# Performance work log

Hardware: AMD Instinct MI355X
Metric: run time of the kernel (lower is better)

Reference implementation:

```python
import jax, jax.numpy as jnp
import numpy as np

B, E, W_WORDS, V = 512, 512, 64, 32000
H = 10 * E  # dense hidden = embedding_size * 10


def setup_inputs() -> dict:
    key = jax.random.key(0)
    ks = jax.random.split(key, 16)
    u = lambda k, shp: jax.random.uniform(ks[k], shp, jnp.float32, -0.05, 0.05)
    n = lambda k, shp: jax.random.normal(ks[k], shp, jnp.float32)
    return {
        "y": n(0, (B, E)),
        "state": n(1, (B, E)),
        "encode": n(2, (B, W_WORDS, E)),
        # Bahdanau attention weights (W4 unused in forward, omitted)
        "aW1": u(3, (1, E)),
        "aW2": u(4, (W_WORDS, E)),
        "aW3": u(5, (W_WORDS, E)),
        # Keras GRU (reset_after=True): kernel, recurrent_kernel, bias[2, 3E]
        "gk": u(6, (E, 3 * E)),
        "grk": u(7, (E, 3 * E)),
        "gb": u(8, (2, 3 * E)),
        # Dense stack
        "w1": u(9, (3 * E, H)), "b1": jnp.zeros((H,), jnp.float32),
        "w2": u(10, (H, H)), "b2": jnp.zeros((H,), jnp.float32),
        "w3": u(11, (H, V)), "b3": jnp.zeros((V,), jnp.float32),
    }


def _attention(query, value, aW1, aW2, aW3):
    # einsum('bi,ci->bi', query, W1) with c==1  ->  query * W1[0]
    rq = query * aW1[0]                       # [B, E]
    rv = value * aW2                          # [B, W, E] (broadcast over batch)
    s = jnp.tanh(rq[:, None, :] * rv)         # [B, W, E]
    scores = jnp.sum(s * aW3, axis=-1)        # [B, W]
    a = jax.nn.softmax(scores, axis=-1)       # [B, W]
    return jnp.einsum('bw,bwe->be', a, value)  # context [B, E]


def _gru(seq, gk, grk, gb):
    # seq: [T, B, E]; keras GRU defaults: tanh / sigmoid, reset_after=True, h0=0
    bi, br = gb[0], gb[1]

    def step(h, x):
        xz, xr, xh = jnp.split(x @ gk + bi, 3, axis=-1)
        rz, rr, rh = jnp.split(h @ grk + br, 3, axis=-1)
        z = jax.nn.sigmoid(xz + rz)
        r = jax.nn.sigmoid(xr + rr)
        hh = jnp.tanh(xh + r * rh)
        return z * h + (1.0 - z) * hh, None

    h0 = jnp.zeros(seq.shape[1:], seq.dtype)
    h, _ = jax.lax.scan(step, h0, seq)
    return h


def reference(y, state, encode, aW1, aW2, aW3, gk, grk, gb, w1, b1, w2, b2, w3, b3):
    context = _attention(state, encode, aW1, aW2, aW3)   # [B, E]
    seq = jnp.stack([state, context, y], axis=0)          # [3, B, E]
    new_state = _gru(seq, gk, grk, gb)                    # [B, E]
    g = jnp.concatenate([y, context, new_state], axis=-1)  # [B, 3E]
    h1 = jnp.tanh(g @ w1 + b1)
    h2 = jnp.tanh(h1 @ w2 + b2)
    g_output = jax.nn.softmax(h2 @ w3 + b3, axis=-1)      # [B, V]
    return (g_output, new_state)
```

## Files before the change

### kernel.cpp

```cpp
#include <hip/hip_runtime.h>
#include <hip/hip_bf16.h>
#include <math.h>

#define B_DIM 512
#define E_DIM 512
#define W_DIM 64
#define V_DIM 32000
#define H_DIM 5120

typedef short bf16x8 __attribute__((ext_vector_type(8)));
typedef float f32x4 __attribute__((ext_vector_type(4)));

static __device__ __forceinline__ unsigned pk2(float a, float b) {
  union { __hip_bfloat16 h; unsigned short u; } ca, cb;
  ca.h = __float2bfloat16(a);
  cb.h = __float2bfloat16(b);
  return (unsigned)ca.u | ((unsigned)cb.u << 16);
}
static __device__ __forceinline__ unsigned short f2b(float a) {
  union { __hip_bfloat16 h; unsigned short u; } c;
  c.h = __float2bfloat16(a);
  return c.u;
}

__global__ __launch_bounds__(256) void attn_kernel(
    const float* __restrict__ state, const float* __restrict__ encode,
    const float* __restrict__ aW1, const float* __restrict__ aW2,
    const float* __restrict__ aW3, float* __restrict__ ctx) {
  const int b = blockIdx.x;
  const int tid = threadIdx.x;
  __shared__ float rq[512];
  __shared__ float sc[64];
  rq[tid]       = state[(size_t)b * 512 + tid]       * aW1[tid];
  rq[tid + 256] = state[(size_t)b * 512 + tid + 256] * aW1[tid + 256];
  __syncthreads();
  const int lane = tid & 63, wv = tid >> 6;
  const float* enc = encode + (size_t)b * 64 * 512;
  for (int w = wv; w < 64; w += 4) {
    const float* er  = enc + w * 512;
    const float* w2r = aW2 + w * 512;
    const float* w3r = aW3 + w * 512;
    float s = 0.f;
#pragma unroll
    for (int k = 0; k < 8; ++k) {
      int e = lane + k * 64;
      s += tanhf(rq[e] * er[e] * w2r[e]) * w3r[e];
    }
#pragma unroll
    for (int o = 32; o; o >>= 1) s += __shfl_xor(s, o, 64);
    if (lane == 0) sc[w] = s;
  }
  __syncthreads();
  if (tid < 64) {
    float v = sc[tid];
    float mx = v;
#pragma unroll
    for (int o = 32; o; o >>= 1) mx = fmaxf(mx, __shfl_xor(mx, o, 64));
    float e = __expf(v - mx);
    float sm = e;
#pragma unroll
    for (int o = 32; o; o >>= 1) sm += __shfl_xor(sm, o, 64);
    sc[tid] = e / sm;
  }
  __syncthreads();
  for (int e = tid; e < 512; e += 256) {
    float acc = 0.f;
#pragma unroll 8
    for (int w = 0; w < 64; ++w) acc += sc[w] * enc[w * 512 + e];
    ctx[(size_t)b * 512 + e] = acc;
  }
}

__global__ __launch_bounds__(256) void pack3b(
    const float* __restrict__ s0, const float* __restrict__ s1,
    const float* __restrict__ s2, unsigned short* __restrict__ dst) {
  const int s = blockIdx.y;
  const int i = blockIdx.x * 256 + threadIdx.x;
  const float* src = (s == 0) ? s0 : ((s == 1) ? s1 : s2);
  const int b = i >> 9, e = i & 511;
  dst[(size_t)b * 1536 + s * 512 + e] = f2b(src[i]);
}

template <int XP, int RP>
__global__ __launch_bounds__(256) void gru_gate(
    const float* __restrict__ X, const float* __restrict__ bi,
    const float* __restrict__ R, const float* __restrict__ br,
    const float* __restrict__ hprev, float* __restrict__ hout) {
  const int i = blockIdx.x * 256 + threadIdx.x;
  const int b = i >> 9, e = i & 511;
  const float* Xr = X + (size_t)b * 1536;
  float xz = bi[e], xr = bi[512 + e], xh = bi[1024 + e];
#pragma unroll
  for (int p = 0; p < XP; ++p) {
    const float* Xp = Xr + (size_t)p * 2359296;
    xz += Xp[e]; xr += Xp[512 + e]; xh += Xp[1024 + e];
  }
  float rz = br[e], rr = br[512 + e], rh = br[1024 + e];
  if (RP > 0) {
    const float* Rr = R + (size_t)b * 1536;
#pragma unroll
    for (int p = 0; p < RP; ++p) {
      const float* Rp = Rr + (size_t)p * 786432;
      rz += Rp[e]; rr += Rp[512 + e]; rh += Rp[1024 + e];
    }
  }
  const float h = hprev ? hprev[i] : 0.f;
  const float z = 1.f / (1.f + __expf(-(xz + rz)));
  const float r = 1.f / (1.f + __expf(-(xr + rr)));
  const float hh = tanhf(xh + r * rh);
  hout[i] = z * h + (1.f - z) * hh;
}

template <int PARTS>
__global__ __launch_bounds__(256, 2) void gemm_k(
    const float* __restrict__ a0, const float* __restrict__ a1,
    const float* __restrict__ a2, const float* __restrict__ B,
    float* __restrict__ C, int M, int N, int K) {
  __shared__ unsigned short As[128 * 72];
  __shared__ unsigned short Bs[128 * 72];
  const int tid = threadIdx.x;
  const int bid = blockIdx.x;
  const int tiles_m = M >> 7;
  const int mt = bid % tiles_m;
  const int nt = bid / tiles_m;
  const long m0 = (long)mt * 128, n0 = (long)nt * 128;
  const int Kp = K / PARTS;
  const int k0 = blockIdx.y * Kp;

  const int a_m = tid & 127;
  const int a_h = tid >> 7;
  unsigned short* awp = As + a_m * 72 + a_h * 32;
  const int b_n = (tid & 31) << 2;
  const int b_q = (tid >> 5) & 3;
  const int b_h = tid >> 7;
  const int b_sw = ((b_q ^ (tid & 3)) << 3) + b_h * 32;

  const int lane = tid & 63;
  const int wid = tid >> 6;
  const int wm = (wid >> 1) << 6, wn = (wid & 1) << 6;
  const int lr = lane & 15, lg = lane >> 4;

  int aro[4], bro[4];
#pragma unroll
  for (int i = 0; i < 4; ++i)
    aro[i] = (wm + 16 * i + lr) * 72 + 8 * lg;
#pragma unroll
  for (int j = 0; j < 4; ++j) {
    const int n = wn + 16 * j + lr;
    bro[j] = n * 72 + 8 * (lg ^ ((n >> 2) & 3));
  }

  f32x4 acc[4][4];
#pragma unroll
  for (int i = 0; i < 4; ++i)
#pragma unroll
    for (int j = 0; j < 4; ++j) acc[i][j] = f32x4{0.f, 0.f, 0.f, 0.f};

  const int row = (int)m0 + a_m;
  const float* asrc = (row < 512) ? a0 : ((row < 1024) ? a1 : a2);
  const float* ap = asrc + (size_t)(row & 511) * 512 + k0 + a_h * 32;
  const float* bp = B + (size_t)(k0 + b_h * 32 + b_q * 8) * N + n0 + b_n;

  float4 pb[8];
#pragma unroll
  for (int j = 0; j < 8; ++j) pb[j] = *(const float4*)(bp + (size_t)j * N);
  bp += (size_t)64 * N;

  const int nsteps = Kp >> 6;
  for (int t = 0; t < nsteps; ++t) {
    float4 pa[8];
#pragma unroll
    for (int j = 0; j < 8; ++j) pa[j] = *(const float4*)(ap + 4 * j);
    ap += 64;
    {
      uint4 w;
      w.x = pk2(pb[0].x, pb[1].x); w.y = pk2(pb[2].x, pb[3].x);
      w.z = pk2(pb[4].x, pb[5].x); w.w = pk2(pb[6].x, pb[7].x);
      *(uint4*)(Bs + (b_n + 0) * 72 + b_sw) = w;
      w.x = pk2(pb[0].y, pb[1].y); w.y = pk2(pb[2].y, pb[3].y);
      w.z = pk2(pb[4].y, pb[5].y); w.w = pk2(pb[6].y, pb[7].y);
      *(uint4*)(Bs + (b_n + 1) * 72 + b_sw) = w;
      w.x = pk2(pb[0].z, pb[1].z); w.y = pk2(pb[2].z, pb[3].z);
      w.z = pk2(pb[4].z, pb[5].z); w.w = pk2(pb[6].z, pb[7].z);
      *(uint4*)(Bs + (b_n + 2) * 72 + b_sw) = w;
      w.x = pk2(pb[0].w, pb[1].w); w.y = pk2(pb[2].w, pb[3].w);
      w.z = pk2(pb[4].w, pb[5].w); w.w = pk2(pb[6].w, pb[7].w);
      *(uint4*)(Bs + (b_n + 3) * 72 + b_sw) = w;
    }
#pragma unroll
    for (int c = 0; c < 4; ++c) {
      uint4 w;
      w.x = pk2(pa[2 * c].x, pa[2 * c].y);
      w.y = pk2(pa[2 * c].z, pa[2 * c].w);
      w.z = pk2(pa[2 * c + 1].x, pa[2 * c + 1].y);
      w.w = pk2(pa[2 * c + 1].z, pa[2 * c + 1].w);
      *(uint4*)(awp + 8 * c) = w;
    }
    __syncthreads();
    if (t + 1 < nsteps) {
#pragma unroll
      for (int j = 0; j < 8; ++j) pb[j] = *(const float4*)(bp + (size_t)j * N);
      bp += (size_t)64 * N;
    }
#pragma unroll
    for (int s = 0; s < 2; ++s) {
      bf16x8 af[4], bfr[4];
#pragma unroll
      for (int i = 0; i < 4; ++i)
        af[i] = *(const bf16x8*)(As + aro[i] + 32 * s);
#pragma unroll
      for (int j = 0; j < 4; ++j)
        bfr[j] = *(const bf16x8*)(Bs + bro[j] + 32 * s);
#pragma unroll
      for (int i = 0; i < 4; ++i)
#pragma unroll
        for (int j = 0; j < 4; ++j)
          acc[i][j] = __builtin_amdgcn_mfma_f32_16x16x32_bf16(af[i], bfr[j], acc[i][j], 0, 0, 0);
    }
    __syncthreads();
  }
  float* Cp = (PARTS > 1) ? (C + (size_t)blockIdx.y * M * (size_t)N) : C;
#pragma unroll
  for (int j = 0; j < 4; ++j) {
    const long col = n0 + wn + j * 16 + lr;
#pragma unroll
    for (int i = 0; i < 4; ++i) {
      const long row2 = m0 + wm + i * 16 + (lg << 2);
#pragma unroll
      for (int r = 0; r < 4; ++r)
        Cp[(row2 + r) * N + col] = acc[i][j][r];
    }
  }
}

template <int ACT, int PARTS>
__global__ __launch_bounds__(512, 2) void gemm_pn(
    const unsigned short* __restrict__ A16, const float* __restrict__ B,
    const float* __restrict__ bias, float* __restrict__ C,
    int N, int K) {
  __shared__ unsigned short Bs[2][128 * 72];
  const int tid = threadIdx.x;
  const long n0 = (long)blockIdx.x * 128;
  const int Kp = K / PARTS;
  const int k0 = blockIdx.y * Kp;

  const int b_x = tid & 31;
  const int b_n = b_x << 2;
  const int b_g = tid >> 5;
  const int b_gs = (((b_g >> 1) ^ ((b_x >> 1) & 7)) << 1) | (b_g & 1);
  const int bw0 = (b_n + 0) * 72 + b_gs * 4;
  const int bw1 = (b_n + 1) * 72 + b_gs * 4;
  const int bw2 = (b_n + 2) * 72 + b_gs * 4;
  const int bw3 = (b_n + 3) * 72 + b_gs * 4;

  const int lane = tid & 63;
  const int wid = tid >> 6;
  const int wm = wid << 6;
  const int lr = lane & 15, lg = lane >> 4;

  int bbase[8], bslot[8];
#pragma unroll
  for (int j = 0; j < 8; ++j) {
    const int n = 16 * j + lr;
    bbase[j] = n * 72;
    bslot[j] = lg ^ ((n >> 3) & 7);
  }

  f32x4 acc[4][8];
#pragma unroll
  for (int i = 0; i < 4; ++i)
#pragma unroll
    for (int j = 0; j < 8; ++j) acc[i][j] = f32x4{0.f, 0.f, 0.f, 0.f};

  const unsigned short* ap0 = A16 + (size_t)(wm + lr) * K + k0 + 8 * lg;
  const unsigned short* ap1 = ap0 + (size_t)16 * K;
  const unsigned short* ap2 = ap0 + (size_t)32 * K;
  const unsigned short* ap3 = ap0 + (size_t)48 * K;
  const float* bp = B + (size_t)(k0 + b_g * 4) * N + n0 + b_n;

  float4 pb0, pb1, pb2, pb3;
  bf16x8 af[8];

#define LOAD_B()                                  \
  do {                                            \
    pb0 = *(const float4*)(bp);                   \
    pb1 = *(const float4*)(bp + N);               \
    pb2 = *(const float4*)(bp + 2 * (size_t)N);   \
    pb3 = *(const float4*)(bp + 3 * (size_t)N);   \
    bp += (size_t)64 * N;                         \
  } while (0)

#define LOAD_A0()                                 \
  do {                                            \
    af[0] = *(const bf16x8*)(ap0);                \
    af[1] = *(const bf16x8*)(ap1);                \
    af[2] = *(const bf16x8*)(ap2);                \
    af[3] = *(const bf16x8*)(ap3);                \
  } while (0)

#define LOAD_A1()                                 \
  do {                                            \
    af[4] = *(const bf16x8*)(ap0 + 32);           \
    af[5] = *(const bf16x8*)(ap1 + 32);           \
    af[6] = *(const bf16x8*)(ap2 + 32);           \
    af[7] = *(const bf16x8*)(ap3 + 32);           \
    ap0 += 64; ap1 += 64; ap2 += 64; ap3 += 64;   \
  } while (0)

#define WRITE_B(buf)                                           \
  do {                                                         \
    uint2 qv;                                                  \
    qv.x = pk2(pb0.x, pb1.x); qv.y = pk2(pb2.x, pb3.x);        \
    *(uint2*)(Bs[buf] + bw0) = qv;                             \
    qv.x = pk2(pb0.y, pb1.y); qv.y = pk2(pb2.y, pb3.y);        \
    *(uint2*)(Bs[buf] + bw1) = qv;                             \
    qv.x = pk2(pb0.z, pb1.z); qv.y = pk2(pb2.z, pb3.z);        \
    *(uint2*)(Bs[buf] + bw2) = qv;                             \
    qv.x = pk2(pb0.w, pb1.w); qv.y = pk2(pb2.w, pb3.w);        \
    *(uint2*)(Bs[buf] + bw3) = qv;                             \
  } while (0)

  const int nsteps = Kp >> 6;
  LOAD_B();
  LOAD_A0();
  LOAD_A1();
  WRITE_B(0);
  LOAD_B();
  asm volatile("s_waitcnt lgkmcnt(0)" ::: "memory");
  __builtin_amdgcn_s_barrier();

  for (int t = 0; t < nsteps; ++t) {
    const int buf = t & 1;
    if (t + 1 < nsteps) { WRITE_B(buf ^ 1); }
    if (t + 2 < nsteps) { LOAD_B(); }
    {
      bf16x8 bfr[8];
#pragma unroll
      for (int j = 0; j < 8; ++j)
        bfr[j] = *(const bf16x8*)(Bs[buf] + bbase[j] + 8 * bslot[j]);
#pragma unroll
      for (int i = 0; i < 4; ++i)
#pragma unroll
        for (int j = 0; j < 8; ++j)
          acc[i][j] = __builtin_amdgcn_mfma_f32_16x16x32_bf16(
              af[i], bfr[j], acc[i][j], 0, 0, 0);
    }
    if (t + 1 < nsteps) { LOAD_A0(); }
    {
      bf16x8 bfr[8];
#pragma unroll
      for (int j = 0; j < 8; ++j)
        bfr[j] = *(const bf16x8*)(Bs[buf] + bbase[j] + 8 * (bslot[j] ^ 4));
#pragma unroll
      for (int i = 0; i < 4; ++i)
#pragma unroll
        for (int j = 0; j < 8; ++j)
          acc[i][j] = __builtin_amdgcn_mfma_f32_16x16x32_bf16(
              af[4 + i], bfr[j], acc[i][j], 0, 0, 0);
    }
    if (t + 1 < nsteps) { LOAD_A1(); }
    asm volatile("s_waitcnt lgkmcnt(0)" ::: "memory");
    __builtin_amdgcn_s_barrier();
  }
#undef LOAD_B
#undef LOAD_A0
#undef LOAD_A1
#undef WRITE_B
  float* Cp = (PARTS > 1) ? (C + (size_t)blockIdx.y * 512 * (size_t)N) : C;
#pragma unroll
  for (int j = 0; j < 8; ++j) {
    const long col = n0 + 16 * j + lr;
    const float bv = (PARTS == 1 && bias) ? bias[col] : 0.f;
#pragma unroll
    for (int i = 0; i < 4; ++i) {
      const long row = wm + 16 * i + (lg << 2);
#pragma unroll
      for (int r = 0; r < 4; ++r) {
        float x = acc[i][j][r] + bv;
        if (PARTS == 1 && ACT == 1) x = tanhf(x);
        Cp[(row + r) * N + col] = x;
      }
    }
  }
}

template <int ACT, int PARTS>
__global__ __launch_bounds__(256) void reduce_parts_b(
    const float* __restrict__ P, const float* __restrict__ bias,
    unsigned short* __restrict__ dst, int N) {
  const int col = blockIdx.x * 256 + threadIdx.x;
  const int row = blockIdx.y;
  const size_t MN = (size_t)512 * N;
  const size_t idx = (size_t)row * N + col;
  float s = bias[col];
#pragma unroll
  for (int p = 0; p < PARTS; ++p) s += P[p * MN + idx];
  dst[idx] = f2b((ACT == 1) ? tanhf(s) : s);
}

__global__ __launch_bounds__(256) void softmax_rows(float* __restrict__ x) {
  const int b = blockIdx.x;
  float* row = x + (size_t)b * V_DIM;
  const int tid = threadIdx.x;
  const int lane = tid & 63, w = tid >> 6;
  __shared__ float sm[4], sl[4];
  const float4* r4 = (const float4*)row;
  float m = -3.4e38f, l = 0.f;
  for (int i = tid; i < V_DIM / 4; i += 256) {
    float4 v = r4[i];
    float cm = fmaxf(fmaxf(v.x, v.y), fmaxf(v.z, v.w));
    if (cm > m) { l *= __expf(m - cm); m = cm; }
    l += __expf(v.x - m) + __expf(v.y - m) + __expf(v.z - m) + __expf(v.w - m);
  }
#pragma unroll
  for (int o = 32; o; o >>= 1) {
    float om = __shfl_xor(m, o, 64);
    float ol = __shfl_xor(l, o, 64);
    float nm = fmaxf(m, om);
    l = l * __expf(m - nm) + ol * __expf(om - nm);
    m = nm;
  }
  if (lane == 0) { sm[w] = m; sl[w] = l; }
  __syncthreads();
  float M = fmaxf(fmaxf(sm[0], sm[1]), fmaxf(sm[2], sm[3]));
  float L = sl[0] * __expf(sm[0] - M) + sl[1] * __expf(sm[1] - M) +
            sl[2] * __expf(sm[2] - M) + sl[3] * __expf(sm[3] - M);
  const float inv = 1.f / L;
  float4* w4p = (float4*)row;
  for (int i = tid; i < V_DIM / 4; i += 256) {
    float4 v = r4[i];
    float4 o4;
    o4.x = __expf(v.x - M) * inv;
    o4.y = __expf(v.y - M) * inv;
    o4.z = __expf(v.z - M) * inv;
    o4.w = __expf(v.w - M) * inv;
    w4p[i] = o4;
  }
}

extern "C" void kernel_launch(void* const* d_in, const int* in_sizes, int n_in,
                              void* d_out, int out_size, void* d_ws, size_t ws_size,
                              hipStream_t stream) {
  const float* y      = (const float*)d_in[0];
  const float* state  = (const float*)d_in[1];
  const float* encode = (const float*)d_in[2];
  const float* aW1    = (const float*)d_in[3];
  const float* aW2    = (const float*)d_in[4];
  const float* aW3    = (const float*)d_in[5];
  const float* gk     = (const float*)d_in[6];
  const float* grk    = (const float*)d_in[7];
  const float* gb     = (const float*)d_in[8];
  const float* w1     = (const float*)d_in[9];
  const float* b1     = (const float*)d_in[10];
  const float* w2     = (const float*)d_in[11];
  const float* b2     = (const float*)d_in[12];
  const float* w3     = (const float*)d_in[13];
  const float* b3     = (const float*)d_in[14];
  float* out = (float*)d_out;
  float* ws = (float*)d_ws;

  float* ctx = ws;
  float* X0  = ws + 262144;
  float* R0  = ws + 9699328;
  float* hg1 = ws + 12845056;
  float* hg2 = ws + 13107200;
  unsigned short* gb16 = (unsigned short*)(ws + 13369344);
  unsigned short* dd1b = (unsigned short*)(ws + 13762560);
  unsigned short* dd2b = (unsigned short*)(ws + 15073280);

  float* g_out = out;
  float* h3 = out + (size_t)B_DIM * V_DIM;
  float* P = out;

  const float* bi = gb;
  const float* br = gb + 1536;

  attn_kernel<<<512, 256, 0, stream>>>(state, encode, aW1, aW2, aW3, ctx);
  gemm_k<4><<<dim3(12 * 12, 4), 256, 0, stream>>>(state, ctx, y, gk, X0, 1536, 1536, 512);
  gru_gate<4, 0><<<1024, 256, 0, stream>>>(X0, bi, nullptr, br, nullptr, hg1);
  gemm_k<4><<<dim3(4 * 12, 4), 256, 0, stream>>>(hg1, hg1, hg1, grk, R0, 512, 1536, 512);
  gru_gate<4, 4><<<1024, 256, 0, stream>>>(X0 + 786432, bi, R0, br, hg1, hg2);
  gemm_k<4><<<dim3(4 * 12, 4), 256, 0, stream>>>(hg2, hg2, hg2, grk, R0, 512, 1536, 512);
  gru_gate<4, 4><<<1024, 256, 0, stream>>>(X0 + 1572864, bi, R0, br, hg2, h3);
  pack3b<<<dim3(1024, 3), 256, 0, stream>>>(y, ctx, h3, gb16);
  gemm_pn<0, 6><<<dim3(40, 6), 512, 0, stream>>>(gb16, w1, nullptr, P, H_DIM, 1536);
  reduce_parts_b<1, 6><<<dim3(20, 512), 256, 0, stream>>>(P, b1, dd1b, H_DIM);
  gemm_pn<0, 5><<<dim3(40, 5), 512, 0, stream>>>(dd1b, w2, nullptr, P, H_DIM, H_DIM);
  reduce_parts_b<1, 5><<<dim3(20, 512), 256, 0, stream>>>(P, b2, dd2b, H_DIM);
  gemm_pn<0, 1><<<dim3(250, 1), 512, 0, stream>>>(dd2b, w3, b3, g_out, V_DIM, H_DIM);
  softmax_rows<<<512, 256, 0, stream>>>(g_out);
}
```

Before: 519.1 us.

## Split final vocab GEMM over K into two parts and fuse reduction into softmax

The output-projection GEMM now runs as a two-way split-K (grid 250x2) writing partial logits to a workspace buffer, instead of one pass over K=5120 with only 250 blocks. The softmax kernel is rewritten to sum the two partials plus bias on the fly in both its max/sum pass and its normalise pass, so no separate reduction kernel is needed. This doubles the number of blocks for the largest GEMM to improve occupancy across CUs. The cost is extra memory traffic: two 65MB partial buffers written and then read twice by softmax. It also assumes the workspace is large enough for the new partial buffer at its offset.

```diff
diff --git a/kernel.cpp b/kernel.cpp
--- a/kernel.cpp
+++ b/kernel.cpp
@@ -398,16 +398,23 @@
   dst[idx] = f2b((ACT == 1) ? tanhf(s) : s);
 }
 
-__global__ __launch_bounds__(256) void softmax_rows(float* __restrict__ x) {
+__global__ __launch_bounds__(256) void softmax_fused(
+    const float* __restrict__ P0, const float* __restrict__ P1,
+    const float* __restrict__ bias, float* __restrict__ outp) {
   const int b = blockIdx.x;
-  float* row = x + (size_t)b * V_DIM;
   const int tid = threadIdx.x;
   const int lane = tid & 63, w = tid >> 6;
   __shared__ float sm[4], sl[4];
-  const float4* r4 = (const float4*)row;
+  const float4* r0 = (const float4*)(P0 + (size_t)b * V_DIM);
+  const float4* r1 = (const float4*)(P1 + (size_t)b * V_DIM);
+  const float4* b4 = (const float4*)bias;
+  float4* w4p = (float4*)(outp + (size_t)b * V_DIM);
   float m = -3.4e38f, l = 0.f;
   for (int i = tid; i < V_DIM / 4; i += 256) {
-    float4 v = r4[i];
+    float4 a = r0[i], c = r1[i], d = b4[i];
+    float4 v;
+    v.x = a.x + c.x + d.x; v.y = a.y + c.y + d.y;
+    v.z = a.z + c.z + d.z; v.w = a.w + c.w + d.w;
     float cm = fmaxf(fmaxf(v.x, v.y), fmaxf(v.z, v.w));
     if (cm > m) { l *= __expf(m - cm); m = cm; }
     l += __expf(v.x - m) + __expf(v.y - m) + __expf(v.z - m) + __expf(v.w - m);
@@ -426,14 +433,13 @@
   float L = sl[0] * __expf(sm[0] - M) + sl[1] * __expf(sm[1] - M) +
             sl[2] * __expf(sm[2] - M) + sl[3] * __expf(sm[3] - M);
   const float inv = 1.f / L;
-  float4* w4p = (float4*)row;
   for (int i = tid; i < V_DIM / 4; i += 256) {
-    float4 v = r4[i];
+    float4 a = r0[i], c = r1[i], d = b4[i];
     float4 o4;
-    o4.x = __expf(v.x - M) * inv;
-    o4.y = __expf(v.y - M) * inv;
-    o4.z = __expf(v.z - M) * inv;
-    o4.w = __expf(v.w - M) * inv;
+    o4.x = __expf(a.x + c.x + d.x - M) * inv;
+    o4.y = __expf(a.y + c.y + d.y - M) * inv;
+    o4.z = __expf(a.z + c.z + d.z - M) * inv;
+    o4.w = __expf(a.w + c.w + d.w - M) * inv;
     w4p[i] = o4;
   }
 }
@@ -467,6 +473,7 @@
   unsigned short* gb16 = (unsigned short*)(ws + 13369344);
   unsigned short* dd1b = (unsigned short*)(ws + 13762560);
   unsigned short* dd2b = (unsigned short*)(ws + 15073280);
+  float* PL = ws + 16777216;
 
   float* g_out = out;
   float* h3 = out + (size_t)B_DIM * V_DIM;
@@ -487,6 +494,6 @@
   reduce_parts_b<1, 6><<<dim3(20, 512), 256, 0, stream>>>(P, b1, dd1b, H_DIM);
   gemm_pn<0, 5><<<dim3(40, 5), 512, 0, stream>>>(dd1b, w2, nullptr, P, H_DIM, H_DIM);
   reduce_parts_b<1, 5><<<dim3(20, 512), 256, 0, stream>>>(P, b2, dd2b, H_DIM);
-  gemm_pn<0, 1><<<dim3(250, 1), 512, 0, stream>>>(dd2b, w3, b3, g_out, V_DIM, H_DIM);
-  softmax_rows<<<512, 256, 0, stream>>>(g_out);
-}
+  gemm_pn<0, 2><<<dim3(250, 2), 512, 0, stream>>>(dd2b, w3, nullptr, PL, V_DIM, H_DIM);
+  softmax_fused<<<512, 256, 0, stream>>>(PL, PL + (size_t)512 * V_DIM, b3, g_out);
+}
```

New measurement: 544.7 us. +4.9%, slower.
